# Optimization experiments

Measured on AMD Instinct MI355X. Metric: run time of the kernel, lower is better.

Reference implementation:

```python
import jax, jax.numpy as jnp
import numpy as np
from jax import lax

B, T, D = 8, 4096, 1024


def setup_inputs() -> dict:
    key = jax.random.key(0)
    ks = jax.random.split(key, 8)
    s = 1.0 / np.sqrt(D)  # keep GEMM outputs O(1)
    return {
        "x": jax.random.normal(ks[0], (B, T, D), dtype=jnp.float32),
        "state_p": jnp.zeros((B, D), dtype=jnp.float32),
        "decay": 0.8 + 0.19 * jax.random.uniform(ks[1], (D,), dtype=jnp.float32),  # ~0.9, stable
        "mass": jnp.ones((D,), dtype=jnp.float32),
        "Wq": s * jax.random.normal(ks[2], (D, D), dtype=jnp.float32),
        "bq": jnp.zeros((D,), dtype=jnp.float32),
        "Wk": s * jax.random.normal(ks[3], (D, D), dtype=jnp.float32),
        "bk": jnp.zeros((D,), dtype=jnp.float32),
        "Wv": s * jax.random.normal(ks[4], (D, D), dtype=jnp.float32),
        "bv": jnp.zeros((D,), dtype=jnp.float32),
    }


def reference(x, state_p, decay, mass, Wq, bq, Wk, bk, Wv, bv):
    # Batch all per-timestep projections into single GEMMs over (B*T) tokens.
    k_logit = jnp.einsum("btd,ed->bte", x, Wk) + bk        # [B,T,D]
    v = jnp.einsum("btd,ed->bte", x, Wv) + bv              # [B,T,D]
    u = jax.nn.sigmoid(k_logit) * v                          # gated input, [B,T,D]

    # Diagonal linear recurrence p_t = decay * p_{t-1} + u_t via scan over time.
    def step(p, u_t):
        p = p * decay + u_t
        return p, p

    final_p, ps = lax.scan(step, state_p, jnp.swapaxes(u, 0, 1))  # ps: [T,B,D]
    p = jnp.swapaxes(ps, 0, 1)                                     # [B,T,D]

    velocities = (jnp.einsum("btd,ed->bte", p, Wq) + bq) / mass    # [B,T,D]
    return velocities, final_p
```

## Files before the change

### kernel.cpp

```cpp
#include <hip/hip_runtime.h>
#include <stdint.h>
#include <stddef.h>

#define D_DIM 1024
#define T_LEN 4096
#define B_SZ 8
#define M_ROWS 32768
#define KTOT 1024
#define CHUNK 128
#define NCHUNK 32

typedef unsigned short u16;
typedef __bf16 bf16x8 __attribute__((ext_vector_type(8)));
typedef float f32x4 __attribute__((ext_vector_type(4)));

__device__ __forceinline__ u16 f2bf(float f) {
    union { float f; unsigned u; } v; v.f = f;
    unsigned r = v.u + 0x7fffu + ((v.u >> 16) & 1u);
    return (u16)(r >> 16);
}
__device__ __forceinline__ float bf2f(u16 h) {
    union { unsigned u; float f; } v; v.u = ((unsigned)h) << 16;
    return v.f;
}

__global__ void convert_kernel(const float* __restrict__ src, u16* __restrict__ dst, int n4) {
    int i = blockIdx.x * blockDim.x + threadIdx.x;
    int stride = gridDim.x * blockDim.x;
    for (int j = i; j < n4; j += stride) {
        float4 v = ((const float4*)src)[j];
        ushort4 o;
        o.x = f2bf(v.x); o.y = f2bf(v.y); o.z = f2bf(v.z); o.w = f2bf(v.w);
        ((ushort4*)dst)[j] = o;
    }
}

__device__ __forceinline__ void gload16(const u16* g, u16* l) {
    __builtin_amdgcn_global_load_lds(
        (const __attribute__((address_space(1))) void*)g,
        (__attribute__((address_space(3))) void*)l,
        16, 0, 0);
}

template<bool DUAL>
__global__ __launch_bounds__(512, 2) void gemm2_kernel(
    const u16* __restrict__ A,
    const u16* __restrict__ B0g,
    const u16* __restrict__ B1g,
    const float* __restrict__ bias0,
    const float* __restrict__ bias1,
    u16* __restrict__ Uout,
    float* __restrict__ Fout)
{
    constexpr int BM = 256;
    constexpr int BN = DUAL ? 128 : 256;
    constexpr int MFR = DUAL ? 4 : 8;
    constexpr int BUF = 16384;
    constexpr int NT = KTOT / 32;

    __shared__ u16 smem[4 * BUF];

    const int tid  = threadIdx.x;
    const int w    = tid >> 6;
    const int lane = tid & 63;

    const int nCol = D_DIM / BN;
    const int M0 = (int)(blockIdx.x / nCol) * BM;
    const int N0 = (int)(blockIdx.x % nCol) * BN;

    const int srow  = lane >> 2;
    const int sslot = lane & 3;
    const int sg    = sslot ^ ((srow >> 1) & 3);

    const u16* pA[2];
    const u16* pB0[2];
    const u16* pB1[1];
#pragma unroll
    for (int ii = 0; ii < 2; ++ii)
        pA[ii] = A + (size_t)(M0 + (w * 2 + ii) * 16 + srow) * KTOT + sg * 8;
    if (DUAL) {
        pB0[0] = B0g + (size_t)(N0 + w * 16 + srow) * KTOT + sg * 8;
        pB1[0] = B1g + (size_t)(N0 + w * 16 + srow) * KTOT + sg * 8;
    } else {
#pragma unroll
        for (int ii = 0; ii < 2; ++ii)
            pB0[ii] = B0g + (size_t)(N0 + (w * 2 + ii) * 16 + srow) * KTOT + sg * 8;
    }

    auto stage = [&](int buf) {
        u16* s = smem + buf * BUF;
#pragma unroll
        for (int ii = 0; ii < 2; ++ii) {
            gload16(pA[ii], s + (w * 2 + ii) * 512);
            pA[ii] += 32;
        }
        if (DUAL) {
            gload16(pB0[0], s + 8192 + w * 512);
            pB0[0] += 32;
            gload16(pB1[0], s + 12288 + w * 512);
            pB1[0] += 32;
        } else {
#pragma unroll
            for (int ii = 0; ii < 2; ++ii) {
                gload16(pB0[ii], s + 8192 + (w * 2 + ii) * 512);
                pB0[ii] += 32;
            }
        }
    };

    const int wrow = DUAL ? (w >> 1) * 64 : (w >> 2) * 128;
    const int wcol = DUAL ? (w & 1) * 64 : (w & 3) * 64;
    const int fr = lane & 15;
    const int fq = lane >> 4;

    int offA[MFR], offB[4];
#pragma unroll
    for (int m = 0; m < MFR; ++m) {
        int row = wrow + m * 16 + fr;
        offA[m] = row * 32 + ((fq ^ ((row >> 1) & 3)) << 3);
    }
#pragma unroll
    for (int n = 0; n < 4; ++n) {
        int row = wcol + n * 16 + fr;
        offB[n] = row * 32 + ((fq ^ ((row >> 1) & 3)) << 3);
    }

    f32x4 acc0[MFR][4] = {};
    f32x4 acc1[MFR][4] = {};

    stage(0); stage(1); stage(2);

    for (int kt = 0; kt < NT; ++kt) {
        if (kt < NT - 2)       asm volatile("s_waitcnt vmcnt(8)" ::: "memory");
        else if (kt == NT - 2) asm volatile("s_waitcnt vmcnt(4)" ::: "memory");
        else                   asm volatile("s_waitcnt vmcnt(0)" ::: "memory");
        __builtin_amdgcn_s_barrier();

        if (kt + 3 < NT) stage((kt + 3) & 3);

        const u16* As  = smem + (kt & 3) * BUF;
        const u16* Bs0 = As + 8192;
        const u16* Bs1 = As + 12288;

        bf16x8 af[MFR], b0f[4], b1f[4];
#pragma unroll
        for (int m = 0; m < MFR; ++m)
            af[m] = *(const bf16x8*)(As + offA[m]);
#pragma unroll
        for (int n = 0; n < 4; ++n) {
            b0f[n] = *(const bf16x8*)(Bs0 + offB[n]);
            if (DUAL) b1f[n] = *(const bf16x8*)(Bs1 + offB[n]);
        }
#pragma unroll
        for (int m = 0; m < MFR; ++m)
#pragma unroll
            for (int n = 0; n < 4; ++n) {
                acc0[m][n] = __builtin_amdgcn_mfma_f32_16x16x32_bf16(af[m], b0f[n], acc0[m][n], 0, 0, 0);
                if (DUAL)
                    acc1[m][n] = __builtin_amdgcn_mfma_f32_16x16x32_bf16(af[m], b1f[n], acc1[m][n], 0, 0, 0);
            }
    }

#pragma unroll
    for (int n = 0; n < 4; ++n) {
        int col = N0 + wcol + n * 16 + fr;
        float b0 = bias0[col];
        float b1 = bias1[col];
#pragma unroll
        for (int m = 0; m < MFR; ++m) {
            int row0 = M0 + wrow + m * 16 + fq * 4;
#pragma unroll
            for (int j = 0; j < 4; ++j) {
                if (DUAL) {
                    float kl = acc0[m][n][j] + b0;
                    float vv = acc1[m][n][j] + b1;
                    float sg2 = 1.0f / (1.0f + __expf(-kl));
                    Uout[(size_t)(row0 + j) * D_DIM + col] = f2bf(sg2 * vv);
                } else {
                    Fout[(size_t)(row0 + j) * D_DIM + col] = (acc0[m][n][j] + b0) / b1;
                }
            }
        }
    }
}

__global__ void chunk_carry_kernel(const u16* __restrict__ u, const float* __restrict__ decay,
                                   float* __restrict__ localc) {
    int id = blockIdx.x * blockDim.x + threadIdx.x;
    int d = id & (D_DIM - 1);
    int c = (id >> 10) & (NCHUNK - 1);
    int b = id >> 15;
    float dec = decay[d];
    const u16* up = u + ((size_t)b * T_LEN + (size_t)c * CHUNK) * D_DIM + d;
    float carry = 0.f;
#pragma unroll 4
    for (int s = 0; s < CHUNK; ++s)
        carry = fmaf(carry, dec, bf2f(up[(size_t)s * D_DIM]));
    localc[id] = carry;
}

__global__ void carry_scan_kernel(const float* __restrict__ localc, const float* __restrict__ state_p,
                                  const float* __restrict__ decay, float* __restrict__ prefix,
                                  float* __restrict__ final_p) {
    int id = blockIdx.x * blockDim.x + threadIdx.x;
    int d = id & (D_DIM - 1);
    int b = id >> 10;
    float dec = decay[d];
    float dl = dec;
#pragma unroll
    for (int i = 0; i < 7; ++i) dl *= dl;
    float P = state_p[id];
    for (int c = 0; c < NCHUNK; ++c) {
        int idx = (b * NCHUNK + c) * D_DIM + d;
        prefix[idx] = P;
        P = fmaf(P, dl, localc[idx]);
    }
    final_p[id] = P;
}

__global__ void reconstruct_kernel(u16* __restrict__ u, const float* __restrict__ decay,
                                   const float* __restrict__ prefix) {
    int id = blockIdx.x * blockDim.x + threadIdx.x;
    int d = id & (D_DIM - 1);
    int c = (id >> 10) & (NCHUNK - 1);
    int b = id >> 15;
    float dec = decay[d];
    float p = prefix[id];
    u16* up = u + ((size_t)b * T_LEN + (size_t)c * CHUNK) * D_DIM + d;
#pragma unroll 4
    for (int s = 0; s < CHUNK; ++s) {
        p = fmaf(p, dec, bf2f(up[(size_t)s * D_DIM]));
        up[(size_t)s * D_DIM] = f2bf(p);
    }
}

extern "C" void kernel_launch(void* const* d_in, const int* in_sizes, int n_in,
                              void* d_out, int out_size, void* d_ws, size_t ws_size,
                              hipStream_t stream) {
    const float* x       = (const float*)d_in[0];
    const float* state_p = (const float*)d_in[1];
    const float* decay   = (const float*)d_in[2];
    const float* mass    = (const float*)d_in[3];
    const float* Wq      = (const float*)d_in[4];
    const float* bq      = (const float*)d_in[5];
    const float* Wk      = (const float*)d_in[6];
    const float* bk      = (const float*)d_in[7];
    const float* Wv      = (const float*)d_in[8];
    const float* bv      = (const float*)d_in[9];

    float* out     = (float*)d_out;
    float* final_p = out + (size_t)M_ROWS * D_DIM;

    u16* xb = (u16*)d_out;

    u16* wkb = (u16*)d_ws;
    u16* wvb = wkb + 1048576;
    u16* wqb = wvb + 1048576;
    u16* ub  = wqb + 1048576;
    float* localc = (float*)(ub + (size_t)M_ROWS * D_DIM);
    float* prefix = localc + B_SZ * NCHUNK * D_DIM;

    convert_kernel<<<4096, 256, 0, stream>>>(x,  xb,  (M_ROWS * D_DIM) / 4);
    convert_kernel<<<1024, 256, 0, stream>>>(Wk, wkb, (D_DIM * D_DIM) / 4);
    convert_kernel<<<1024, 256, 0, stream>>>(Wv, wvb, (D_DIM * D_DIM) / 4);
    convert_kernel<<<1024, 256, 0, stream>>>(Wq, wqb, (D_DIM * D_DIM) / 4);

    gemm2_kernel<true><<<dim3(1024), dim3(512), 0, stream>>>(
        xb, wkb, wvb, bk, bv, ub, nullptr);

    chunk_carry_kernel<<<1024, 256, 0, stream>>>(ub, decay, localc);
    carry_scan_kernel<<<32, 256, 0, stream>>>(localc, state_p, decay, prefix, final_p);
    reconstruct_kernel<<<1024, 256, 0, stream>>>(ub, decay, prefix);

    gemm2_kernel<false><<<dim3(512), dim3(512), 0, stream>>>(
        ub, wqb, nullptr, bq, mass, nullptr, out);
}
```

Baseline: 318.7 us.

## Split GEMM K-step into interleaved halves, swizzle blocks, vectorize chunked scan

The GEMM main loop now splits each K-step into two MFMA phases, issuing A and B prefetches between them with priority raising and schedule barriers, and remaps block IDs for better L2 reuse. The scan kernels are vectorized to handle 8 channels per thread with 16-byte loads and stores, and the chunk size drops to 64 with more chunks. The three weight conversions are merged into one launch. The extra barrier per K-step and reduced thread count in the scan kernels may offset some gains.

```diff
diff --git a/kernel.cpp b/kernel.cpp
--- a/kernel.cpp
+++ b/kernel.cpp
@@ -7,10 +7,11 @@
 #define B_SZ 8
 #define M_ROWS 32768
 #define KTOT 1024
-#define CHUNK 128
-#define NCHUNK 32
+#define CHUNK 64
+#define NCHUNK 64
 
 typedef unsigned short u16;
+typedef unsigned short u16x8 __attribute__((ext_vector_type(8)));
 typedef __bf16 bf16x8 __attribute__((ext_vector_type(8)));
 typedef float f32x4 __attribute__((ext_vector_type(4)));
 
@@ -35,6 +36,25 @@
     }
 }
 
+__global__ void convert3_kernel(const float* __restrict__ s0, const float* __restrict__ s1,
+                                const float* __restrict__ s2,
+                                u16* __restrict__ d0, u16* __restrict__ d1, u16* __restrict__ d2,
+                                int n4each) {
+    int i = blockIdx.x * blockDim.x + threadIdx.x;
+    int total = 3 * n4each;
+    int stride = gridDim.x * blockDim.x;
+    for (int j = i; j < total; j += stride) {
+        int which = j / n4each;
+        int off = j - which * n4each;
+        const float* s = which == 0 ? s0 : (which == 1 ? s1 : s2);
+        u16* d = which == 0 ? d0 : (which == 1 ? d1 : d2);
+        float4 v = ((const float4*)s)[off];
+        ushort4 o;
+        o.x = f2bf(v.x); o.y = f2bf(v.y); o.z = f2bf(v.z); o.w = f2bf(v.w);
+        ((ushort4*)d)[off] = o;
+    }
+}
+
 __device__ __forceinline__ void gload16(const u16* g, u16* l) {
     __builtin_amdgcn_global_load_lds(
         (const __attribute__((address_space(1))) void*)g,
@@ -43,7 +63,7 @@
 }
 
 template<bool DUAL>
-__global__ __launch_bounds__(512, 2) void gemm2_kernel(
+__global__ __launch_bounds__(512, 2) void gemm3_kernel(
     const u16* __restrict__ A,
     const u16* __restrict__ B0g,
     const u16* __restrict__ B1g,
@@ -64,47 +84,44 @@
     const int w    = tid >> 6;
     const int lane = tid & 63;
 
+    const int cpx = gridDim.x >> 3;
+    const int bid = blockIdx.x;
+    const int swz = (bid & 7) * cpx + (bid >> 3);
+
     const int nCol = D_DIM / BN;
-    const int M0 = (int)(blockIdx.x / nCol) * BM;
-    const int N0 = (int)(blockIdx.x % nCol) * BN;
+    const int M0 = (swz / nCol) * BM;
+    const int N0 = (swz % nCol) * BM / (BM / BN);
 
     const int srow  = lane >> 2;
     const int sslot = lane & 3;
     const int sg    = sslot ^ ((srow >> 1) & 3);
 
-    const u16* pA[2];
-    const u16* pB0[2];
-    const u16* pB1[1];
-#pragma unroll
-    for (int ii = 0; ii < 2; ++ii)
-        pA[ii] = A + (size_t)(M0 + (w * 2 + ii) * 16 + srow) * KTOT + sg * 8;
+    const u16* pA0 = A + (size_t)(M0 + (w * 2 + 0) * 16 + srow) * KTOT + sg * 8;
+    const u16* pA1 = A + (size_t)(M0 + (w * 2 + 1) * 16 + srow) * KTOT + sg * 8;
+    const u16* pB0a;
+    const u16* pB0b = nullptr;
+    const u16* pB1a = nullptr;
     if (DUAL) {
-        pB0[0] = B0g + (size_t)(N0 + w * 16 + srow) * KTOT + sg * 8;
-        pB1[0] = B1g + (size_t)(N0 + w * 16 + srow) * KTOT + sg * 8;
+        pB0a = B0g + (size_t)(N0 + w * 16 + srow) * KTOT + sg * 8;
+        pB1a = B1g + (size_t)(N0 + w * 16 + srow) * KTOT + sg * 8;
     } else {
-#pragma unroll
-        for (int ii = 0; ii < 2; ++ii)
-            pB0[ii] = B0g + (size_t)(N0 + (w * 2 + ii) * 16 + srow) * KTOT + sg * 8;
-    }
-
-    auto stage = [&](int buf) {
+        pB0a = B0g + (size_t)(N0 + (w * 2 + 0) * 16 + srow) * KTOT + sg * 8;
+        pB0b = B0g + (size_t)(N0 + (w * 2 + 1) * 16 + srow) * KTOT + sg * 8;
+    }
+
+    auto stageA = [&](int buf) {
         u16* s = smem + buf * BUF;
-#pragma unroll
-        for (int ii = 0; ii < 2; ++ii) {
-            gload16(pA[ii], s + (w * 2 + ii) * 512);
-            pA[ii] += 32;
-        }
+        gload16(pA0, s + (w * 2 + 0) * 512); pA0 += 32;
+        gload16(pA1, s + (w * 2 + 1) * 512); pA1 += 32;
+    };
+    auto stageB = [&](int buf) {
+        u16* s = smem + buf * BUF;
         if (DUAL) {
-            gload16(pB0[0], s + 8192 + w * 512);
-            pB0[0] += 32;
-            gload16(pB1[0], s + 12288 + w * 512);
-            pB1[0] += 32;
+            gload16(pB0a, s + 8192 + w * 512);  pB0a += 32;
+            gload16(pB1a, s + 12288 + w * 512); pB1a += 32;
         } else {
-#pragma unroll
-            for (int ii = 0; ii < 2; ++ii) {
-                gload16(pB0[ii], s + 8192 + (w * 2 + ii) * 512);
-                pB0[ii] += 32;
-            }
+            gload16(pB0a, s + 8192 + (w * 2 + 0) * 512); pB0a += 32;
+            gload16(pB0b, s + 8192 + (w * 2 + 1) * 512); pB0b += 32;
         }
     };
 
@@ -126,9 +143,9 @@
     }
 
     f32x4 acc0[MFR][4] = {};
-    f32x4 acc1[MFR][4] = {};
-
-    stage(0); stage(1); stage(2);
+    f32x4 acc1[DUAL ? MFR : 1][4] = {};
+
+    stageA(0); stageB(0); stageA(1); stageB(1); stageA(2); stageB(2);
 
     for (int kt = 0; kt < NT; ++kt) {
         if (kt < NT - 2)       asm volatile("s_waitcnt vmcnt(8)" ::: "memory");
@@ -136,29 +153,59 @@
         else                   asm volatile("s_waitcnt vmcnt(0)" ::: "memory");
         __builtin_amdgcn_s_barrier();
 
-        if (kt + 3 < NT) stage((kt + 3) & 3);
-
         const u16* As  = smem + (kt & 3) * BUF;
         const u16* Bs0 = As + 8192;
         const u16* Bs1 = As + 12288;
 
         bf16x8 af[MFR], b0f[4], b1f[4];
-#pragma unroll
-        for (int m = 0; m < MFR; ++m)
+
+#pragma unroll
+        for (int m = 0; m < 4; ++m)
             af[m] = *(const bf16x8*)(As + offA[m]);
 #pragma unroll
-        for (int n = 0; n < 4; ++n) {
+        for (int n = 0; n < 4; ++n)
             b0f[n] = *(const bf16x8*)(Bs0 + offB[n]);
-            if (DUAL) b1f[n] = *(const bf16x8*)(Bs1 + offB[n]);
-        }
-#pragma unroll
-        for (int m = 0; m < MFR; ++m)
-#pragma unroll
-            for (int n = 0; n < 4; ++n) {
+        if (kt + 3 < NT) stageA((kt + 3) & 3);
+        asm volatile("s_waitcnt lgkmcnt(0)" ::: "memory");
+        __builtin_amdgcn_sched_barrier(0);
+        __builtin_amdgcn_s_setprio(1);
+#pragma unroll
+        for (int m = 0; m < 4; ++m)
+#pragma unroll
+            for (int n = 0; n < 4; ++n)
                 acc0[m][n] = __builtin_amdgcn_mfma_f32_16x16x32_bf16(af[m], b0f[n], acc0[m][n], 0, 0, 0);
-                if (DUAL)
+        __builtin_amdgcn_s_setprio(0);
+        __builtin_amdgcn_sched_barrier(0);
+
+        __builtin_amdgcn_s_barrier();
+        if (DUAL) {
+#pragma unroll
+            for (int n = 0; n < 4; ++n)
+                b1f[n] = *(const bf16x8*)(Bs1 + offB[n]);
+        } else {
+#pragma unroll
+            for (int m = 4; m < MFR; ++m)
+                af[m] = *(const bf16x8*)(As + offA[m]);
+        }
+        if (kt + 3 < NT) stageB((kt + 3) & 3);
+        asm volatile("s_waitcnt lgkmcnt(0)" ::: "memory");
+        __builtin_amdgcn_sched_barrier(0);
+        __builtin_amdgcn_s_setprio(1);
+        if (DUAL) {
+#pragma unroll
+            for (int m = 0; m < 4; ++m)
+#pragma unroll
+                for (int n = 0; n < 4; ++n)
                     acc1[m][n] = __builtin_amdgcn_mfma_f32_16x16x32_bf16(af[m], b1f[n], acc1[m][n], 0, 0, 0);
-            }
+        } else {
+#pragma unroll
+            for (int m = 4; m < MFR; ++m)
+#pragma unroll
+                for (int n = 0; n < 4; ++n)
+                    acc0[m][n] = __builtin_amdgcn_mfma_f32_16x16x32_bf16(af[m], b0f[n], acc0[m][n], 0, 0, 0);
+        }
+        __builtin_amdgcn_s_setprio(0);
+        __builtin_amdgcn_sched_barrier(0);
     }
 
 #pragma unroll
@@ -187,16 +234,23 @@
 __global__ void chunk_carry_kernel(const u16* __restrict__ u, const float* __restrict__ decay,
                                    float* __restrict__ localc) {
     int id = blockIdx.x * blockDim.x + threadIdx.x;
-    int d = id & (D_DIM - 1);
-    int c = (id >> 10) & (NCHUNK - 1);
-    int b = id >> 15;
-    float dec = decay[d];
-    const u16* up = u + ((size_t)b * T_LEN + (size_t)c * CHUNK) * D_DIM + d;
-    float carry = 0.f;
-#pragma unroll 4
-    for (int s = 0; s < CHUNK; ++s)
-        carry = fmaf(carry, dec, bf2f(up[(size_t)s * D_DIM]));
-    localc[id] = carry;
+    int d8 = id & 127;
+    int c  = (id >> 7) & (NCHUNK - 1);
+    int b  = id >> 13;
+    float4 dlo = ((const float4*)decay)[d8 * 2];
+    float4 dhi = ((const float4*)decay)[d8 * 2 + 1];
+    float dec[8] = {dlo.x, dlo.y, dlo.z, dlo.w, dhi.x, dhi.y, dhi.z, dhi.w};
+    float carry[8] = {};
+    const u16* up = u + ((size_t)b * T_LEN + (size_t)c * CHUNK) * D_DIM + d8 * 8;
+    for (int s = 0; s < CHUNK; ++s) {
+        u16x8 v = *(const u16x8*)(up + (size_t)s * D_DIM);
+#pragma unroll
+        for (int j = 0; j < 8; ++j)
+            carry[j] = fmaf(carry[j], dec[j], bf2f(v[j]));
+    }
+    float* lc = localc + ((size_t)(b * NCHUNK + c)) * D_DIM + d8 * 8;
+#pragma unroll
+    for (int j = 0; j < 8; ++j) lc[j] = carry[j];
 }
 
 __global__ void carry_scan_kernel(const float* __restrict__ localc, const float* __restrict__ state_p,
@@ -208,7 +262,7 @@
     float dec = decay[d];
     float dl = dec;
 #pragma unroll
-    for (int i = 0; i < 7; ++i) dl *= dl;
+    for (int i = 0; i < 6; ++i) dl *= dl;
     float P = state_p[id];
     for (int c = 0; c < NCHUNK; ++c) {
         int idx = (b * NCHUNK + c) * D_DIM + d;
@@ -221,16 +275,26 @@
 __global__ void reconstruct_kernel(u16* __restrict__ u, const float* __restrict__ decay,
                                    const float* __restrict__ prefix) {
     int id = blockIdx.x * blockDim.x + threadIdx.x;
-    int d = id & (D_DIM - 1);
-    int c = (id >> 10) & (NCHUNK - 1);
-    int b = id >> 15;
-    float dec = decay[d];
-    float p = prefix[id];
-    u16* up = u + ((size_t)b * T_LEN + (size_t)c * CHUNK) * D_DIM + d;
-#pragma unroll 4
+    int d8 = id & 127;
+    int c  = (id >> 7) & (NCHUNK - 1);
+    int b  = id >> 13;
+    float4 dlo = ((const float4*)decay)[d8 * 2];
+    float4 dhi = ((const float4*)decay)[d8 * 2 + 1];
+    float dec[8] = {dlo.x, dlo.y, dlo.z, dlo.w, dhi.x, dhi.y, dhi.z, dhi.w};
+    const float* pf = prefix + ((size_t)(b * NCHUNK + c)) * D_DIM + d8 * 8;
+    float p[8];
+#pragma unroll
+    for (int j = 0; j < 8; ++j) p[j] = pf[j];
+    u16* up = u + ((size_t)b * T_LEN + (size_t)c * CHUNK) * D_DIM + d8 * 8;
     for (int s = 0; s < CHUNK; ++s) {
-        p = fmaf(p, dec, bf2f(up[(size_t)s * D_DIM]));
-        up[(size_t)s * D_DIM] = f2bf(p);
+        u16x8 v = *(const u16x8*)(up + (size_t)s * D_DIM);
+        u16x8 o;
+#pragma unroll
+        for (int j = 0; j < 8; ++j) {
+            p[j] = fmaf(p[j], dec[j], bf2f(v[j]));
+            o[j] = f2bf(p[j]);
+        }
+        *(u16x8*)(up + (size_t)s * D_DIM) = o;
     }
 }
 
@@ -260,18 +324,16 @@
     float* localc = (float*)(ub + (size_t)M_ROWS * D_DIM);
     float* prefix = localc + B_SZ * NCHUNK * D_DIM;
 
-    convert_kernel<<<4096, 256, 0, stream>>>(x,  xb,  (M_ROWS * D_DIM) / 4);
-    convert_kernel<<<1024, 256, 0, stream>>>(Wk, wkb, (D_DIM * D_DIM) / 4);
-    convert_kernel<<<1024, 256, 0, stream>>>(Wv, wvb, (D_DIM * D_DIM) / 4);
-    convert_kernel<<<1024, 256, 0, stream>>>(Wq, wqb, (D_DIM * D_DIM) / 4);
-
-    gemm2_kernel<true><<<dim3(1024), dim3(512), 0, stream>>>(
+    convert_kernel<<<4096, 256, 0, stream>>>(x, xb, (M_ROWS * D_DIM) / 4);
+    convert3_kernel<<<1024, 256, 0, stream>>>(Wk, Wv, Wq, wkb, wvb, wqb, (D_DIM * D_DIM) / 4);
+
+    gemm3_kernel<true><<<dim3(1024), dim3(512), 0, stream>>>(
         xb, wkb, wvb, bk, bv, ub, nullptr);
 
-    chunk_carry_kernel<<<1024, 256, 0, stream>>>(ub, decay, localc);
+    chunk_carry_kernel<<<256, 256, 0, stream>>>(ub, decay, localc);
     carry_scan_kernel<<<32, 256, 0, stream>>>(localc, state_p, decay, prefix, final_p);
-    reconstruct_kernel<<<1024, 256, 0, stream>>>(ub, decay, prefix);
-
-    gemm2_kernel<false><<<dim3(512), dim3(512), 0, stream>>>(
+    reconstruct_kernel<<<256, 256, 0, stream>>>(ub, decay, prefix);
+
+    gemm3_kernel<false><<<dim3(512), dim3(512), 0, stream>>>(
         ub, wqb, nullptr, bq, mass, nullptr, out);
 }
```

Measured after the change: 306.4 us. 1.04x faster.
